# Optimization experiments

Measured on AMD Instinct MI355X. Metric: run time of the kernel, lower is better.

Reference implementation:

```python
import jax, jax.numpy as jnp
import numpy as np

N = 100000        # number of graph nodes
IN_DIM = 256      # input feature dim
OUT_DIM = 64      # output feature dim
X_NNZ = 1_600_000 # nnz of sparse feature matrix x (avg 16 per node)
A_NNZ = 3_200_000 # nnz of sparse adjacency (avg degree 32)
KEEP_PROB = 0.9   # 1 - dropout


def setup_inputs() -> dict:
    key = jax.random.key(0)
    ks = jax.random.split(key, 8)
    x_vals = jax.random.normal(ks[0], (X_NNZ,), dtype=jnp.float32)
    x_rows = jax.random.randint(ks[1], (X_NNZ,), 0, N, dtype=jnp.int32)
    x_cols = jax.random.randint(ks[2], (X_NNZ,), 0, IN_DIM, dtype=jnp.int32)
    adj_vals = jax.random.uniform(ks[3], (A_NNZ,), dtype=jnp.float32)
    adj_rows = jax.random.randint(ks[4], (A_NNZ,), 0, N, dtype=jnp.int32)
    adj_cols = jax.random.randint(ks[5], (A_NNZ,), 0, N, dtype=jnp.int32)
    # Glorot uniform init, as in weight_variable_glorot
    lim = float(np.sqrt(6.0 / (IN_DIM + OUT_DIM)))
    W = jax.random.uniform(ks[6], (IN_DIM, OUT_DIM), dtype=jnp.float32, minval=-lim, maxval=lim)
    # deterministic dropout retain mask (Bernoulli(keep_prob)), mirrors dropout_sparse
    keep_mask = jax.random.uniform(ks[7], (X_NNZ,)) < KEEP_PROB
    return {
        "x_vals": x_vals, "x_rows": x_rows, "x_cols": x_cols,
        "adj_vals": adj_vals, "adj_rows": adj_rows, "adj_cols": adj_cols,
        "W": W, "keep_mask": keep_mask,
    }


def reference(x_vals, x_rows, x_cols, adj_vals, adj_rows, adj_cols, W, keep_mask):
    # sparse dropout: retain + rescale by 1/keep_prob
    xv = jnp.where(keep_mask, x_vals, jnp.float32(0.0)) * jnp.float32(1.0 / KEEP_PROB)
    # spmm 1: h = x @ W  -> gather W rows by feature col index, scatter-add by node row
    h = jax.ops.segment_sum(xv[:, None] * W[x_cols], x_rows, num_segments=N)  # [N, OUT_DIM]
    # spmm 2: agg = adj @ h -> gather neighbor features, scatter-add by destination node
    agg = jax.ops.segment_sum(adj_vals[:, None] * h[adj_cols], adj_rows, num_segments=N)  # [N, OUT_DIM]
    return jax.nn.relu(agg)
```

## Files before the change

### kernel.cpp

```cpp
#include <hip/hip_runtime.h>
#include <hip/hip_bf16.h>

#define N_NODES 100000
#define IN_DIM 256
#define OUT_DIM 64
#define INV_KEEP 1.1111111111111112f

#define BROWS 256
#define NBUCKET ((N_NODES + BROWS - 1) / BROWS)
#define BCPAD 16
#define A_CAP 9728
#define X_CAP 5120

#define PART_BLOCKS 256

__device__ __forceinline__ int   ldnt (const int* p)   { return __builtin_nontemporal_load(p); }
__device__ __forceinline__ float ldntf(const float* p) { return __builtin_nontemporal_load(p); }


__global__ __launch_bounds__(256) void bucket_hist_kernel(
    const int* __restrict__ rows, const int* __restrict__ keep,
    int* __restrict__ bcnt, int nnz)
{
    __shared__ int cnt[NBUCKET];
    const int chunk = (nnz + (int)gridDim.x - 1) / (int)gridDim.x;
    const int lo = (int)blockIdx.x * chunk;
    const int hi = min(lo + chunk, nnz);

    for (int k = threadIdx.x; k < NBUCKET; k += blockDim.x) cnt[k] = 0;
    __syncthreads();
    if (keep) {
        for (int e = lo + (int)threadIdx.x; e < hi; e += (int)blockDim.x)
            if (ldnt(keep + e) != 0) atomicAdd(&cnt[ldnt(rows + e) >> 8], 1);
    } else {
        for (int e = lo + (int)threadIdx.x; e < hi; e += (int)blockDim.x)
            atomicAdd(&cnt[ldnt(rows + e) >> 8], 1);
    }
    __syncthreads();
    for (int k = threadIdx.x; k < NBUCKET; k += blockDim.x) {
        int n = cnt[k];
        if (n > 0) atomicAdd(&bcnt[k], n);
    }
}


__global__ __launch_bounds__(512) void bucket_scan_kernel(
    const int* __restrict__ bcnt_x, const int* __restrict__ bcnt_a,
    int* __restrict__ bstart_x, int* __restrict__ bstart_a,
    int* __restrict__ bcurx, int* __restrict__ bcura)
{
    const int* c  = blockIdx.x ? bcnt_a : bcnt_x;
    int* bs       = blockIdx.x ? bstart_a : bstart_x;
    int* bc       = blockIdx.x ? bcura : bcurx;
    __shared__ int sc[512];
    const int t = threadIdx.x;
    sc[t] = (t < NBUCKET) ? c[t] : 0;
    __syncthreads();
    for (int off = 1; off < 512; off <<= 1) {
        int v = (t >= off) ? sc[t - off] : 0;
        __syncthreads();
        sc[t] += v;
        __syncthreads();
    }
    if (t < NBUCKET) {
        int excl = (t > 0) ? sc[t - 1] : 0;
        bs[t] = excl;
        bc[t * BCPAD] = excl;
        if (t == NBUCKET - 1) bs[NBUCKET] = sc[t];
    }
}


__global__ __launch_bounds__(256) void partition_x_kernel(
    const float* __restrict__ xv, const int* __restrict__ xr,
    const int* __restrict__ xc, const int* __restrict__ keep,
    int* __restrict__ bcur, float2* __restrict__ out, int nnz)
{
    __shared__ int cnt[NBUCKET];
    const int chunk = (nnz + (int)gridDim.x - 1) / (int)gridDim.x;
    const int lo = (int)blockIdx.x * chunk;
    const int hi = min(lo + chunk, nnz);

    for (int k = threadIdx.x; k < NBUCKET; k += blockDim.x) cnt[k] = 0;
    __syncthreads();
    for (int e = lo + (int)threadIdx.x; e < hi; e += (int)blockDim.x)
        if (ldnt(keep + e) != 0) atomicAdd(&cnt[ldnt(xr + e) >> 8], 1);
    __syncthreads();
    for (int k = threadIdx.x; k < NBUCKET; k += blockDim.x) {
        int n = cnt[k];
        cnt[k] = (n > 0) ? atomicAdd(&bcur[k * BCPAD], n) : 0;
    }
    __syncthreads();
    for (int e = lo + (int)threadIdx.x; e < hi; e += (int)blockDim.x) {
        if (ldnt(keep + e) == 0) continue;
        int r = ldnt(xr + e);
        int c = ldnt(xc + e);
        float v = ldntf(xv + e) * INV_KEEP;
        int pos = atomicAdd(&cnt[r >> 8], 1);
        out[pos] = make_float2(v, __uint_as_float(((unsigned)c << 8) | (unsigned)(r & (BROWS - 1))));
    }
}

__global__ __launch_bounds__(256) void partition_a_kernel(
    const float* __restrict__ av, const int* __restrict__ ar,
    const int* __restrict__ ac,
    int* __restrict__ bcur, float2* __restrict__ out, int nnz)
{
    __shared__ int cnt[NBUCKET];
    const int chunk = (nnz + (int)gridDim.x - 1) / (int)gridDim.x;
    const int lo = (int)blockIdx.x * chunk;
    const int hi = min(lo + chunk, nnz);

    for (int k = threadIdx.x; k < NBUCKET; k += blockDim.x) cnt[k] = 0;
    __syncthreads();
    for (int e = lo + (int)threadIdx.x; e < hi; e += (int)blockDim.x)
        atomicAdd(&cnt[ldnt(ar + e) >> 8], 1);
    __syncthreads();
    for (int k = threadIdx.x; k < NBUCKET; k += blockDim.x) {
        int n = cnt[k];
        cnt[k] = (n > 0) ? atomicAdd(&bcur[k * BCPAD], n) : 0;
    }
    __syncthreads();
    for (int e = lo + (int)threadIdx.x; e < hi; e += (int)blockDim.x) {
        int r = ldnt(ar + e);
        int c = ldnt(ac + e);
        float v = ldntf(av + e);
        int pos = atomicAdd(&cnt[r >> 8], 1);
        out[pos] = make_float2(v, __uint_as_float(((unsigned)c << 8) | (unsigned)(r & (BROWS - 1))));
    }
}


template <int CAP>
__global__ __launch_bounds__(256) void reorder_kernel(
    const int* __restrict__ bstart, float2* __restrict__ data,
    int* __restrict__ start)
{
    __shared__ float2 recs[CAP];
    __shared__ int rcnt[BROWS];
    __shared__ int sc[BROWS];
    __shared__ int curs[BROWS];
    const int b = blockIdx.x;
    const int brow0 = b * BROWS;
    const int rows_n = min(BROWS, N_NODES - brow0);
    const int base = bstart[b];
    int size = bstart[b + 1] - base;
    if (size > CAP) size = CAP;
    const int t = threadIdx.x;

    rcnt[t] = 0;
    __syncthreads();
    for (int i = t; i < size; i += 256) {
        float2 rec = data[base + i];
        recs[i] = rec;
        atomicAdd(&rcnt[__float_as_uint(rec.y) & (BROWS - 1)], 1);
    }
    __syncthreads();
    sc[t] = rcnt[t];
    __syncthreads();
    for (int off = 1; off < 256; off <<= 1) {
        int v = (t >= off) ? sc[t - off] : 0;
        __syncthreads();
        sc[t] += v;
        __syncthreads();
    }
    int excl = (t > 0) ? sc[t - 1] : 0;
    curs[t] = base + excl;
    if (t < rows_n) start[brow0 + t] = base + excl;
    if (brow0 + rows_n == N_NODES && t == rows_n - 1) start[N_NODES] = base + size;
    __syncthreads();
    for (int i = t; i < size; i += 256) {
        float2 rec = recs[i];
        unsigned u = __float_as_uint(rec.y);
        int pos = atomicAdd(&curs[u & (BROWS - 1)], 1);
        data[pos] = make_float2(rec.x, __int_as_float((int)(u >> 8)));
    }
}


__global__ __launch_bounds__(256) void spmm1_csr_kernel(
    const int* __restrict__ xs_start, const float2* __restrict__ xs,
    const float* __restrict__ W, __hip_bfloat16* __restrict__ h)
{
    const int wave = (int)((blockIdx.x * blockDim.x + threadIdx.x) >> 6);
    const int lane = threadIdx.x & 63;
    if (wave >= N_NODES) return;

    const int s = xs_start[wave];
    const int e = xs_start[wave + 1];
    float acc = 0.0f;
    int j = s;
    for (; j + 4 <= e; j += 4) {
        float2 p0 = xs[j + 0];
        float2 p1 = xs[j + 1];
        float2 p2 = xs[j + 2];
        float2 p3 = xs[j + 3];
        float g0 = W[__float_as_int(p0.y) * OUT_DIM + lane];
        float g1 = W[__float_as_int(p1.y) * OUT_DIM + lane];
        float g2 = W[__float_as_int(p2.y) * OUT_DIM + lane];
        float g3 = W[__float_as_int(p3.y) * OUT_DIM + lane];
        acc += p0.x * g0;
        acc += p1.x * g1;
        acc += p2.x * g2;
        acc += p3.x * g3;
    }
    for (; j < e; ++j) {
        float2 p = xs[j];
        acc += p.x * W[__float_as_int(p.y) * OUT_DIM + lane];
    }
    h[(size_t)wave * OUT_DIM + lane] = __float2bfloat16(acc);
}

__global__ __launch_bounds__(256) void spmm2_csr_kernel(
    const int* __restrict__ as_start, const float2* __restrict__ as,
    const __hip_bfloat16* __restrict__ h, float* __restrict__ out)
{
    const int wave = (int)((blockIdx.x * blockDim.x + threadIdx.x) >> 6);
    const int lane = threadIdx.x & 63;
    if (wave >= N_NODES) return;

    const int s = as_start[wave];
    const int e = as_start[wave + 1];
    float acc = 0.0f;
    int j = s;
    for (; j + 8 <= e; j += 8) {
        float2 p0 = as[j + 0];
        float2 p1 = as[j + 1];
        float2 p2 = as[j + 2];
        float2 p3 = as[j + 3];
        float2 p4 = as[j + 4];
        float2 p5 = as[j + 5];
        float2 p6 = as[j + 6];
        float2 p7 = as[j + 7];
        float g0 = __bfloat162float(h[(size_t)__float_as_int(p0.y) * OUT_DIM + lane]);
        float g1 = __bfloat162float(h[(size_t)__float_as_int(p1.y) * OUT_DIM + lane]);
        float g2 = __bfloat162float(h[(size_t)__float_as_int(p2.y) * OUT_DIM + lane]);
        float g3 = __bfloat162float(h[(size_t)__float_as_int(p3.y) * OUT_DIM + lane]);
        float g4 = __bfloat162float(h[(size_t)__float_as_int(p4.y) * OUT_DIM + lane]);
        float g5 = __bfloat162float(h[(size_t)__float_as_int(p5.y) * OUT_DIM + lane]);
        float g6 = __bfloat162float(h[(size_t)__float_as_int(p6.y) * OUT_DIM + lane]);
        float g7 = __bfloat162float(h[(size_t)__float_as_int(p7.y) * OUT_DIM + lane]);
        acc += p0.x * g0;
        acc += p1.x * g1;
        acc += p2.x * g2;
        acc += p3.x * g3;
        acc += p4.x * g4;
        acc += p5.x * g5;
        acc += p6.x * g6;
        acc += p7.x * g7;
    }
    for (; j < e; ++j) {
        float2 p = as[j];
        acc += p.x * __bfloat162float(h[(size_t)__float_as_int(p.y) * OUT_DIM + lane]);
    }
    out[(size_t)wave * OUT_DIM + lane] = acc > 0.0f ? acc : 0.0f;
}


__global__ __launch_bounds__(256) void spmm1_atomic_kernel(
    const float* __restrict__ x_vals, const int* __restrict__ x_rows,
    const int* __restrict__ x_cols, const int* __restrict__ keep,
    const float* __restrict__ W, float* __restrict__ h, int nnz)
{
    const int lane   = threadIdx.x & 63;
    const int group  = (int)((blockIdx.x * blockDim.x + threadIdx.x) >> 6);
    const int stride = (int)((gridDim.x * blockDim.x) >> 6);
    for (int e = group; e < nnz; e += stride) {
        float v = (keep[e] != 0) ? x_vals[e] * INV_KEEP : 0.0f;
        if (v != 0.0f)
            atomicAdd(&h[(size_t)x_rows[e] * OUT_DIM + lane],
                      v * W[x_cols[e] * OUT_DIM + lane]);
    }
}

__global__ __launch_bounds__(256) void spmm2_atomic_kernel(
    const float* __restrict__ adj_vals, const int* __restrict__ adj_rows,
    const int* __restrict__ adj_cols, const float* __restrict__ h,
    float* __restrict__ out, int nnz)
{
    const int lane   = threadIdx.x & 63;
    const int group  = (int)((blockIdx.x * blockDim.x + threadIdx.x) >> 6);
    const int stride = (int)((gridDim.x * blockDim.x) >> 6);
    for (int e = group; e < nnz; e += stride) {
        atomicAdd(&out[(size_t)adj_rows[e] * OUT_DIM + lane],
                  adj_vals[e] * h[(size_t)adj_cols[e] * OUT_DIM + lane]);
    }
}

__global__ __launch_bounds__(256) void relu_kernel(float* __restrict__ out, int n)
{
    int i = (int)(blockIdx.x * blockDim.x + threadIdx.x);
    if (i < n) {
        float v = out[i];
        out[i] = v > 0.0f ? v : 0.0f;
    }
}


extern "C" void kernel_launch(void* const* d_in, const int* in_sizes, int n_in,
                              void* d_out, int out_size, void* d_ws, size_t ws_size,
                              hipStream_t stream)
{
    const float* x_vals   = (const float*)d_in[0];
    const int*   x_rows   = (const int*)d_in[1];
    const int*   x_cols   = (const int*)d_in[2];
    const float* adj_vals = (const float*)d_in[3];
    const int*   adj_rows = (const int*)d_in[4];
    const int*   adj_cols = (const int*)d_in[5];
    const float* W        = (const float*)d_in[6];
    const int*   keep     = (const int*)d_in[7];

    const int x_nnz = in_sizes[0];
    const int a_nnz = in_sizes[3];

    float* out = (float*)d_out;

    char* ws = (char*)d_ws;
    size_t off = 0;
    float2* xs = (float2*)(ws + off);            off += (size_t)x_nnz * 8;
    float2* as = (float2*)(ws + off);            off += (size_t)a_nnz * 8;
    __hip_bfloat16* hb = (__hip_bfloat16*)(ws + off); off += (size_t)N_NODES * OUT_DIM * 2;
    int* x_start  = (int*)(ws + off);            off += (size_t)(N_NODES + 1) * 4;
    int* a_start  = (int*)(ws + off);            off += (size_t)(N_NODES + 1) * 4;
    int* bcnt_x   = (int*)(ws + off);            off += (size_t)NBUCKET * 4;
    int* bcnt_a   = (int*)(ws + off);            off += (size_t)NBUCKET * 4;
    int* bstart_x = (int*)(ws + off);            off += (size_t)(NBUCKET + 1) * 4;
    int* bstart_a = (int*)(ws + off);            off += (size_t)(NBUCKET + 1) * 4;
    int* bcurx    = (int*)(ws + off);            off += (size_t)NBUCKET * BCPAD * 4;
    int* bcura    = (int*)(ws + off);            off += (size_t)NBUCKET * BCPAD * 4;
    const size_t needed = off;

    if (ws_size >= needed) {
        hipMemsetAsync(bcnt_x, 0, (size_t)2 * NBUCKET * 4, stream);

        bucket_hist_kernel<<<512, 256, 0, stream>>>(x_rows, keep, bcnt_x, x_nnz);
        bucket_hist_kernel<<<512, 256, 0, stream>>>(adj_rows, (const int*)nullptr, bcnt_a, a_nnz);

        bucket_scan_kernel<<<2, 512, 0, stream>>>(bcnt_x, bcnt_a, bstart_x, bstart_a,
                                                  bcurx, bcura);

        partition_x_kernel<<<PART_BLOCKS, 256, 0, stream>>>(x_vals, x_rows, x_cols, keep,
                                                            bcurx, xs, x_nnz);
        partition_a_kernel<<<PART_BLOCKS, 256, 0, stream>>>(adj_vals, adj_rows, adj_cols,
                                                            bcura, as, a_nnz);

        reorder_kernel<X_CAP><<<NBUCKET, 256, 0, stream>>>(bstart_x, xs, x_start);
        reorder_kernel<A_CAP><<<NBUCKET, 256, 0, stream>>>(bstart_a, as, a_start);

        const int blocks = (N_NODES * 64 + 255) / 256;
        spmm1_csr_kernel<<<blocks, 256, 0, stream>>>(x_start, xs, W, hb);
        spmm2_csr_kernel<<<blocks, 256, 0, stream>>>(a_start, as, hb, out);
    } else {
        float* hf = (float*)d_ws;
        hipMemsetAsync(hf, 0, (size_t)N_NODES * OUT_DIM * 4, stream);
        hipMemsetAsync(out, 0, (size_t)out_size * 4, stream);
        spmm1_atomic_kernel<<<4096, 256, 0, stream>>>(x_vals, x_rows, x_cols, keep, W, hf, x_nnz);
        spmm2_atomic_kernel<<<4096, 256, 0, stream>>>(adj_vals, adj_rows, adj_cols, hf, out, a_nnz);
        relu_kernel<<<(out_size + 255) / 256, 256, 0, stream>>>(out, out_size);
    }
}
```

Before: 374.1 us.

## Precompute per-block bucket offsets via column scan and fuse x/adj partition passes

Replaces the global-atomic partitioning with a deterministic three-pass scheme. Per-block bucket histograms are stored and column-scanned to give each block its own base offsets, so the partition kernel no longer re-counts its chunk or takes global atomics. The x and adjacency histogram and placement kernels are merged into single launches and the memset is dropped. Record-stream loads and the output stores in the SpMM kernels are also made nontemporal. The cost is an extra colscan launch and a per-block count matrix in global memory.

```diff
diff --git a/kernel.cpp b/kernel.cpp
--- a/kernel.cpp
+++ b/kernel.cpp
@@ -8,128 +8,128 @@
 
 #define BROWS 256
 #define NBUCKET ((N_NODES + BROWS - 1) / BROWS)
-#define BCPAD 16
+#define PBLK 256
 #define A_CAP 9728
 #define X_CAP 5120
 
-#define PART_BLOCKS 256
-
 __device__ __forceinline__ int   ldnt (const int* p)   { return __builtin_nontemporal_load(p); }
 __device__ __forceinline__ float ldntf(const float* p) { return __builtin_nontemporal_load(p); }
-
-
-__global__ __launch_bounds__(256) void bucket_hist_kernel(
-    const int* __restrict__ rows, const int* __restrict__ keep,
-    int* __restrict__ bcnt, int nnz)
+__device__ __forceinline__ float2 ldnt2(const float2* p) {
+    double d = __builtin_nontemporal_load(reinterpret_cast<const double*>(p));
+    union { double d; float2 f; } u; u.d = d; return u.f;
+}
+__device__ __forceinline__ void stnt_bf16(__hip_bfloat16* p, __hip_bfloat16 v) {
+    __builtin_nontemporal_store(*reinterpret_cast<unsigned short*>(&v),
+                                reinterpret_cast<unsigned short*>(p));
+}
+
+__global__ __launch_bounds__(256) void hist_count_kernel(
+    const int* __restrict__ xr, const int* __restrict__ keep,
+    const int* __restrict__ ar,
+    int* __restrict__ cnt_blk_x, int* __restrict__ cnt_blk_a,
+    int x_nnz, int a_nnz)
 {
     __shared__ int cnt[NBUCKET];
-    const int chunk = (nnz + (int)gridDim.x - 1) / (int)gridDim.x;
-    const int lo = (int)blockIdx.x * chunk;
-    const int hi = min(lo + chunk, nnz);
-
-    for (int k = threadIdx.x; k < NBUCKET; k += blockDim.x) cnt[k] = 0;
-    __syncthreads();
-    if (keep) {
-        for (int e = lo + (int)threadIdx.x; e < hi; e += (int)blockDim.x)
-            if (ldnt(keep + e) != 0) atomicAdd(&cnt[ldnt(rows + e) >> 8], 1);
+    const bool isA = blockIdx.x >= PBLK;
+    const int ib = isA ? (int)blockIdx.x - PBLK : (int)blockIdx.x;
+    const int nnz = isA ? a_nnz : x_nnz;
+    const int chunk = (nnz + PBLK - 1) / PBLK;
+    const int lo = ib * chunk, hi = min(lo + chunk, nnz);
+
+    for (int k = threadIdx.x; k < NBUCKET; k += 256) cnt[k] = 0;
+    __syncthreads();
+    if (isA) {
+        for (int e = lo + (int)threadIdx.x; e < hi; e += 256)
+            atomicAdd(&cnt[ldnt(ar + e) >> 8], 1);
     } else {
-        for (int e = lo + (int)threadIdx.x; e < hi; e += (int)blockDim.x)
-            atomicAdd(&cnt[ldnt(rows + e) >> 8], 1);
-    }
-    __syncthreads();
-    for (int k = threadIdx.x; k < NBUCKET; k += blockDim.x) {
-        int n = cnt[k];
-        if (n > 0) atomicAdd(&bcnt[k], n);
-    }
-}
-
+        for (int e = lo + (int)threadIdx.x; e < hi; e += 256)
+            if (ldnt(keep + e) != 0) atomicAdd(&cnt[ldnt(xr + e) >> 8], 1);
+    }
+    __syncthreads();
+    int* dst = (isA ? cnt_blk_a : cnt_blk_x) + (size_t)ib * NBUCKET;
+    for (int k = threadIdx.x; k < NBUCKET; k += 256) dst[k] = cnt[k];
+}
+
+__global__ __launch_bounds__(256) void colscan_kernel(
+    int* __restrict__ cnt_blk_x, int* __restrict__ cnt_blk_a,
+    int* __restrict__ btot_x, int* __restrict__ btot_a)
+{
+    const bool isA = blockIdx.x >= NBUCKET;
+    const int k = isA ? (int)blockIdx.x - NBUCKET : (int)blockIdx.x;
+    int* cb = isA ? cnt_blk_a : cnt_blk_x;
+    __shared__ int sc[PBLK];
+    const int t = threadIdx.x;
+    int v = cb[(size_t)t * NBUCKET + k];
+    sc[t] = v;
+    __syncthreads();
+    for (int off = 1; off < PBLK; off <<= 1) {
+        int u = (t >= off) ? sc[t - off] : 0;
+        __syncthreads();
+        sc[t] += u;
+        __syncthreads();
+    }
+    cb[(size_t)t * NBUCKET + k] = sc[t] - v;
+    if (t == PBLK - 1) (isA ? btot_a : btot_x)[k] = sc[t];
+}
 
 __global__ __launch_bounds__(512) void bucket_scan_kernel(
-    const int* __restrict__ bcnt_x, const int* __restrict__ bcnt_a,
-    int* __restrict__ bstart_x, int* __restrict__ bstart_a,
-    int* __restrict__ bcurx, int* __restrict__ bcura)
-{
-    const int* c  = blockIdx.x ? bcnt_a : bcnt_x;
-    int* bs       = blockIdx.x ? bstart_a : bstart_x;
-    int* bc       = blockIdx.x ? bcura : bcurx;
+    const int* __restrict__ btot_x, const int* __restrict__ btot_a,
+    int* __restrict__ bstart_x, int* __restrict__ bstart_a)
+{
+    const int* c = blockIdx.x ? btot_a : btot_x;
+    int* bs      = blockIdx.x ? bstart_a : bstart_x;
     __shared__ int sc[512];
     const int t = threadIdx.x;
     sc[t] = (t < NBUCKET) ? c[t] : 0;
     __syncthreads();
     for (int off = 1; off < 512; off <<= 1) {
-        int v = (t >= off) ? sc[t - off] : 0;
-        __syncthreads();
-        sc[t] += v;
-        __syncthreads();
-    }
-    if (t < NBUCKET) {
-        int excl = (t > 0) ? sc[t - 1] : 0;
-        bs[t] = excl;
-        bc[t * BCPAD] = excl;
-        if (t == NBUCKET - 1) bs[NBUCKET] = sc[t];
-    }
-}
-
-
-__global__ __launch_bounds__(256) void partition_x_kernel(
+        int u = (t >= off) ? sc[t - off] : 0;
+        __syncthreads();
+        sc[t] += u;
+        __syncthreads();
+    }
+    if (t < NBUCKET) bs[t] = (t > 0) ? sc[t - 1] : 0;
+    if (t == NBUCKET - 1) bs[NBUCKET] = sc[t];
+}
+
+__global__ __launch_bounds__(256) void partition_place_kernel(
     const float* __restrict__ xv, const int* __restrict__ xr,
     const int* __restrict__ xc, const int* __restrict__ keep,
-    int* __restrict__ bcur, float2* __restrict__ out, int nnz)
-{
-    __shared__ int cnt[NBUCKET];
-    const int chunk = (nnz + (int)gridDim.x - 1) / (int)gridDim.x;
-    const int lo = (int)blockIdx.x * chunk;
-    const int hi = min(lo + chunk, nnz);
-
-    for (int k = threadIdx.x; k < NBUCKET; k += blockDim.x) cnt[k] = 0;
-    __syncthreads();
-    for (int e = lo + (int)threadIdx.x; e < hi; e += (int)blockDim.x)
-        if (ldnt(keep + e) != 0) atomicAdd(&cnt[ldnt(xr + e) >> 8], 1);
-    __syncthreads();
-    for (int k = threadIdx.x; k < NBUCKET; k += blockDim.x) {
-        int n = cnt[k];
-        cnt[k] = (n > 0) ? atomicAdd(&bcur[k * BCPAD], n) : 0;
-    }
-    __syncthreads();
-    for (int e = lo + (int)threadIdx.x; e < hi; e += (int)blockDim.x) {
-        if (ldnt(keep + e) == 0) continue;
-        int r = ldnt(xr + e);
-        int c = ldnt(xc + e);
-        float v = ldntf(xv + e) * INV_KEEP;
-        int pos = atomicAdd(&cnt[r >> 8], 1);
-        out[pos] = make_float2(v, __uint_as_float(((unsigned)c << 8) | (unsigned)(r & (BROWS - 1))));
-    }
-}
-
-__global__ __launch_bounds__(256) void partition_a_kernel(
     const float* __restrict__ av, const int* __restrict__ ar,
     const int* __restrict__ ac,
-    int* __restrict__ bcur, float2* __restrict__ out, int nnz)
-{
-    __shared__ int cnt[NBUCKET];
-    const int chunk = (nnz + (int)gridDim.x - 1) / (int)gridDim.x;
-    const int lo = (int)blockIdx.x * chunk;
-    const int hi = min(lo + chunk, nnz);
-
-    for (int k = threadIdx.x; k < NBUCKET; k += blockDim.x) cnt[k] = 0;
-    __syncthreads();
-    for (int e = lo + (int)threadIdx.x; e < hi; e += (int)blockDim.x)
-        atomicAdd(&cnt[ldnt(ar + e) >> 8], 1);
-    __syncthreads();
-    for (int k = threadIdx.x; k < NBUCKET; k += blockDim.x) {
-        int n = cnt[k];
-        cnt[k] = (n > 0) ? atomicAdd(&bcur[k * BCPAD], n) : 0;
-    }
-    __syncthreads();
-    for (int e = lo + (int)threadIdx.x; e < hi; e += (int)blockDim.x) {
-        int r = ldnt(ar + e);
-        int c = ldnt(ac + e);
-        float v = ldntf(av + e);
-        int pos = atomicAdd(&cnt[r >> 8], 1);
-        out[pos] = make_float2(v, __uint_as_float(((unsigned)c << 8) | (unsigned)(r & (BROWS - 1))));
-    }
-}
-
+    const int* __restrict__ cnt_blk_x, const int* __restrict__ cnt_blk_a,
+    const int* __restrict__ bstart_x, const int* __restrict__ bstart_a,
+    float2* __restrict__ xs, float2* __restrict__ as, int x_nnz, int a_nnz)
+{
+    __shared__ int off_l[NBUCKET];
+    const bool isA = blockIdx.x >= PBLK;
+    const int ib = isA ? (int)blockIdx.x - PBLK : (int)blockIdx.x;
+    const int nnz = isA ? a_nnz : x_nnz;
+    const int chunk = (nnz + PBLK - 1) / PBLK;
+    const int lo = ib * chunk, hi = min(lo + chunk, nnz);
+    const int* cb = (isA ? cnt_blk_a : cnt_blk_x) + (size_t)ib * NBUCKET;
+    const int* bs = isA ? bstart_a : bstart_x;
+    float2* out   = isA ? as : xs;
+
+    for (int k = threadIdx.x; k < NBUCKET; k += 256) off_l[k] = bs[k] + cb[k];
+    __syncthreads();
+    if (isA) {
+        for (int e = lo + (int)threadIdx.x; e < hi; e += 256) {
+            int r = ldnt(ar + e), c = ldnt(ac + e);
+            float v = ldntf(av + e);
+            int pos = atomicAdd(&off_l[r >> 8], 1);
+            out[pos] = make_float2(v, __uint_as_float(((unsigned)c << 8) | (unsigned)(r & (BROWS - 1))));
+        }
+    } else {
+        for (int e = lo + (int)threadIdx.x; e < hi; e += 256) {
+            if (ldnt(keep + e) == 0) continue;
+            int r = ldnt(xr + e), c = ldnt(xc + e);
+            float v = ldntf(xv + e) * INV_KEEP;
+            int pos = atomicAdd(&off_l[r >> 8], 1);
+            out[pos] = make_float2(v, __uint_as_float(((unsigned)c << 8) | (unsigned)(r & (BROWS - 1))));
+        }
+    }
+}
 
 template <int CAP>
 __global__ __launch_bounds__(256) void reorder_kernel(
@@ -191,10 +191,10 @@
     float acc = 0.0f;
     int j = s;
     for (; j + 4 <= e; j += 4) {
-        float2 p0 = xs[j + 0];
-        float2 p1 = xs[j + 1];
-        float2 p2 = xs[j + 2];
-        float2 p3 = xs[j + 3];
+        float2 p0 = ldnt2(xs + j + 0);
+        float2 p1 = ldnt2(xs + j + 1);
+        float2 p2 = ldnt2(xs + j + 2);
+        float2 p3 = ldnt2(xs + j + 3);
         float g0 = W[__float_as_int(p0.y) * OUT_DIM + lane];
         float g1 = W[__float_as_int(p1.y) * OUT_DIM + lane];
         float g2 = W[__float_as_int(p2.y) * OUT_DIM + lane];
@@ -205,10 +205,10 @@
         acc += p3.x * g3;
     }
     for (; j < e; ++j) {
-        float2 p = xs[j];
+        float2 p = ldnt2(xs + j);
         acc += p.x * W[__float_as_int(p.y) * OUT_DIM + lane];
     }
-    h[(size_t)wave * OUT_DIM + lane] = __float2bfloat16(acc);
+    stnt_bf16(&h[(size_t)wave * OUT_DIM + lane], __float2bfloat16(acc));
 }
 
 __global__ __launch_bounds__(256) void spmm2_csr_kernel(
@@ -224,14 +224,14 @@
     float acc = 0.0f;
     int j = s;
     for (; j + 8 <= e; j += 8) {
-        float2 p0 = as[j + 0];
-        float2 p1 = as[j + 1];
-        float2 p2 = as[j + 2];
-        float2 p3 = as[j + 3];
-        float2 p4 = as[j + 4];
-        float2 p5 = as[j + 5];
-        float2 p6 = as[j + 6];
-        float2 p7 = as[j + 7];
+        float2 p0 = ldnt2(as + j + 0);
+        float2 p1 = ldnt2(as + j + 1);
+        float2 p2 = ldnt2(as + j + 2);
+        float2 p3 = ldnt2(as + j + 3);
+        float2 p4 = ldnt2(as + j + 4);
+        float2 p5 = ldnt2(as + j + 5);
+        float2 p6 = ldnt2(as + j + 6);
+        float2 p7 = ldnt2(as + j + 7);
         float g0 = __bfloat162float(h[(size_t)__float_as_int(p0.y) * OUT_DIM + lane]);
         float g1 = __bfloat162float(h[(size_t)__float_as_int(p1.y) * OUT_DIM + lane]);
         float g2 = __bfloat162float(h[(size_t)__float_as_int(p2.y) * OUT_DIM + lane]);
@@ -250,10 +250,11 @@
         acc += p7.x * g7;
     }
     for (; j < e; ++j) {
-        float2 p = as[j];
+        float2 p = ldnt2(as + j);
         acc += p.x * __bfloat162float(h[(size_t)__float_as_int(p.y) * OUT_DIM + lane]);
     }
-    out[(size_t)wave * OUT_DIM + lane] = acc > 0.0f ? acc : 0.0f;
+    float r = acc > 0.0f ? acc : 0.0f;
+    __builtin_nontemporal_store(r, &out[(size_t)wave * OUT_DIM + lane]);
 }
 
 
@@ -317,32 +318,32 @@
 
     char* ws = (char*)d_ws;
     size_t off = 0;
-    float2* xs = (float2*)(ws + off);            off += (size_t)x_nnz * 8;
-    float2* as = (float2*)(ws + off);            off += (size_t)a_nnz * 8;
+    float2* xs = (float2*)(ws + off);                 off += (size_t)x_nnz * 8;
+    float2* as = (float2*)(ws + off);                 off += (size_t)a_nnz * 8;
     __hip_bfloat16* hb = (__hip_bfloat16*)(ws + off); off += (size_t)N_NODES * OUT_DIM * 2;
-    int* x_start  = (int*)(ws + off);            off += (size_t)(N_NODES + 1) * 4;
-    int* a_start  = (int*)(ws + off);            off += (size_t)(N_NODES + 1) * 4;
-    int* bcnt_x   = (int*)(ws + off);            off += (size_t)NBUCKET * 4;
-    int* bcnt_a   = (int*)(ws + off);            off += (size_t)NBUCKET * 4;
-    int* bstart_x = (int*)(ws + off);            off += (size_t)(NBUCKET + 1) * 4;
-    int* bstart_a = (int*)(ws + off);            off += (size_t)(NBUCKET + 1) * 4;
-    int* bcurx    = (int*)(ws + off);            off += (size_t)NBUCKET * BCPAD * 4;
-    int* bcura    = (int*)(ws + off);            off += (size_t)NBUCKET * BCPAD * 4;
+    int* x_start   = (int*)(ws + off);                off += (size_t)(N_NODES + 1) * 4;
+    int* a_start   = (int*)(ws + off);                off += (size_t)(N_NODES + 1) * 4;
+    int* cnt_blk_x = (int*)(ws + off);                off += (size_t)PBLK * NBUCKET * 4;
+    int* cnt_blk_a = (int*)(ws + off);                off += (size_t)PBLK * NBUCKET * 4;
+    int* btot_x    = (int*)(ws + off);                off += (size_t)NBUCKET * 4;
+    int* btot_a    = (int*)(ws + off);                off += (size_t)NBUCKET * 4;
+    int* bstart_x  = (int*)(ws + off);                off += (size_t)(NBUCKET + 1) * 4;
+    int* bstart_a  = (int*)(ws + off);                off += (size_t)(NBUCKET + 1) * 4;
     const size_t needed = off;
 
     if (ws_size >= needed) {
-        hipMemsetAsync(bcnt_x, 0, (size_t)2 * NBUCKET * 4, stream);
-
-        bucket_hist_kernel<<<512, 256, 0, stream>>>(x_rows, keep, bcnt_x, x_nnz);
-        bucket_hist_kernel<<<512, 256, 0, stream>>>(adj_rows, (const int*)nullptr, bcnt_a, a_nnz);
-
-        bucket_scan_kernel<<<2, 512, 0, stream>>>(bcnt_x, bcnt_a, bstart_x, bstart_a,
-                                                  bcurx, bcura);
-
-        partition_x_kernel<<<PART_BLOCKS, 256, 0, stream>>>(x_vals, x_rows, x_cols, keep,
-                                                            bcurx, xs, x_nnz);
-        partition_a_kernel<<<PART_BLOCKS, 256, 0, stream>>>(adj_vals, adj_rows, adj_cols,
-                                                            bcura, as, a_nnz);
+        hist_count_kernel<<<2 * PBLK, 256, 0, stream>>>(
+            x_rows, keep, adj_rows, cnt_blk_x, cnt_blk_a, x_nnz, a_nnz);
+
+        colscan_kernel<<<2 * NBUCKET, 256, 0, stream>>>(
+            cnt_blk_x, cnt_blk_a, btot_x, btot_a);
+
+        bucket_scan_kernel<<<2, 512, 0, stream>>>(
+            btot_x, btot_a, bstart_x, bstart_a);
+
+        partition_place_kernel<<<2 * PBLK, 256, 0, stream>>>(
+            x_vals, x_rows, x_cols, keep, adj_vals, adj_rows, adj_cols,
+            cnt_blk_x, cnt_blk_a, bstart_x, bstart_a, xs, as, x_nnz, a_nnz);
 
         reorder_kernel<X_CAP><<<NBUCKET, 256, 0, stream>>>(bstart_x, xs, x_start);
         reorder_kernel<A_CAP><<<NBUCKET, 256, 0, stream>>>(bstart_a, as, a_start);
```

New measurement: 335.4 us. 1.12x faster.
